# Performance work log

Measured on AMD Instinct MI355X. Metric: run time of the kernel, lower is better.

The kernel has to match this reference:

```python
import jax, jax.numpy as jnp
import numpy as np

N = 100000      # num nodes
E = 1600000     # num edges
D_IN = 128
D_OUT = 64
PRELU_INIT = 0.25


def setup_inputs() -> dict:
    key = jax.random.key(0)
    k1, k2, k3, k4, k5 = jax.random.split(key, 5)
    node_x = jax.random.normal(k1, (N, D_IN), dtype=jnp.float32)
    edge_rows = jax.random.randint(k2, (E,), 0, N, dtype=jnp.int32)
    edge_cols = jax.random.randint(k3, (E,), 0, N, dtype=jnp.int32)
    edge_vals = jax.random.uniform(k4, (E,), dtype=jnp.float32)
    # Xavier-uniform init for weights
    limit = float(np.sqrt(6.0 / (D_IN + D_OUT)))
    weights = jax.random.uniform(k5, (D_IN, D_OUT), dtype=jnp.float32,
                                 minval=-limit, maxval=limit)
    prelu_a = jnp.float32(PRELU_INIT)
    return {"node_x": node_x, "edge_rows": edge_rows, "edge_cols": edge_cols,
            "edge_vals": edge_vals, "weights": weights, "prelu_a": prelu_a}


def reference(node_x, edge_rows, edge_cols, edge_vals, weights, prelu_a):
    # Dense projection: [N, D_IN] @ [D_IN, D_OUT] -> [N, D_OUT]
    support = jnp.matmul(node_x, weights)
    # Sparse-dense matmul: output[r] = sum_{(r,c,v) in adj} v * support[c]
    messages = edge_vals[:, None] * support[edge_cols]  # [E, D_OUT]
    output = jax.ops.segment_sum(messages, edge_rows, num_segments=N)
    # PReLU with single learned scalar
    out = jnp.where(output > 0, output, prelu_a * output)
    return (out, support)
```

## Files before the change

kernel.cpp:

```cpp
#include <hip/hip_runtime.h>

#define N_NODES 100000
#define N_EDGES 1600000
#define D_IN    128
#define D_OUT   64

#define XT_STRIDE 260
#define NBUCKETS 1563
#define NBW 782
#define G 392
#define SLICE 4096
#define M_FLAT (NBUCKETS * G)
#define SCANA_BLOCKS 599
#define GEMM_BLOCKS 391
#define CAP 2048
typedef unsigned long long ull;
typedef unsigned int uint;

__global__ __launch_bounds__(256) void k_gemm_cnt(
    const float* __restrict__ x,
    const float* __restrict__ w,
    float* __restrict__ support,
    const int* __restrict__ rows,
    uint* __restrict__ S)
{
    __shared__ float wl[D_IN * D_OUT];
    __shared__ float xT[32 * XT_STRIDE];

    const int t = threadIdx.x;

    if (blockIdx.x >= GEMM_BLOCKS) {
        uint* hist = (uint*)wl;
        const int bid = blockIdx.x - GEMM_BLOCKS;
        const int b = (bid & 7) * 49 + (bid >> 3);
        for (int i = t; i < NBW; i += 256) hist[i] = 0u;
        __syncthreads();

        const int base = b * SLICE;
#pragma unroll
        for (int s2 = 0; s2 < 4; ++s2) {
            const int e = base + s2 * 1024 + t * 4;
            if (e < N_EDGES) {
                const int4 r4 = *(const int4*)&rows[e];
                atomicAdd(&hist[(uint)r4.x >> 7], 1u << ((((uint)r4.x >> 6) & 1) * 16));
                atomicAdd(&hist[(uint)r4.y >> 7], 1u << ((((uint)r4.y >> 6) & 1) * 16));
                atomicAdd(&hist[(uint)r4.z >> 7], 1u << ((((uint)r4.z >> 6) & 1) * 16));
                atomicAdd(&hist[(uint)r4.w >> 7], 1u << ((((uint)r4.w >> 6) & 1) * 16));
            }
        }
        __syncthreads();

        for (int i = t; i < NBUCKETS; i += 256)
            S[(size_t)i * G + b] = (hist[i >> 1] >> ((i & 1) * 16)) & 0xffffu;
        return;
    }

    const int tx = t & 7;
    const int ty = t >> 3;
    const long row0 = (long)blockIdx.x * 256;

    {
        const float4* wf  = (const float4*)w;
        float4*       wlf = (float4*)wl;
#pragma unroll
        for (int j = 0; j < 8; ++j)
            wlf[t + 256 * j] = wf[t + 256 * j];
    }

    float acc[8][8];
#pragma unroll
    for (int i = 0; i < 8; ++i)
#pragma unroll
        for (int j = 0; j < 8; ++j)
            acc[i][j] = 0.f;

    for (int kc = 0; kc < 4; ++kc) {
        const int k0 = kc * 32;
        __syncthreads();

        const int kk = tx * 4;
#pragma unroll
        for (int it = 0; it < 8; ++it) {
            const int  rg   = it * 32 + ty;
            const long grow = row0 + rg;
            float4 v = make_float4(0.f, 0.f, 0.f, 0.f);
            if (grow < N_NODES)
                v = *(const float4*)&x[grow * D_IN + k0 + kk];
            xT[(kk + 0) * XT_STRIDE + rg] = v.x;
            xT[(kk + 1) * XT_STRIDE + rg] = v.y;
            xT[(kk + 2) * XT_STRIDE + rg] = v.z;
            xT[(kk + 3) * XT_STRIDE + rg] = v.w;
        }
        __syncthreads();

#pragma unroll 8
        for (int k = 0; k < 32; ++k) {
            const float4 a0 = *(const float4*)&xT[k * XT_STRIDE + ty * 8];
            const float4 a1 = *(const float4*)&xT[k * XT_STRIDE + ty * 8 + 4];
            const float4 b0 = *(const float4*)&wl[(k0 + k) * D_OUT + tx * 8];
            const float4 b1 = *(const float4*)&wl[(k0 + k) * D_OUT + tx * 8 + 4];
            const float av[8] = {a0.x, a0.y, a0.z, a0.w, a1.x, a1.y, a1.z, a1.w};
            const float bv[8] = {b0.x, b0.y, b0.z, b0.w, b1.x, b1.y, b1.z, b1.w};
#pragma unroll
            for (int i = 0; i < 8; ++i)
#pragma unroll
                for (int j = 0; j < 8; ++j)
                    acc[i][j] = fmaf(av[i], bv[j], acc[i][j]);
        }
    }

#pragma unroll
    for (int i = 0; i < 8; ++i) {
        const long r = row0 + ty * 8 + i;
        if (r < N_NODES) {
            float4 o0 = make_float4(acc[i][0], acc[i][1], acc[i][2], acc[i][3]);
            float4 o1 = make_float4(acc[i][4], acc[i][5], acc[i][6], acc[i][7]);
            *(float4*)&support[r * D_OUT + tx * 8]     = o0;
            *(float4*)&support[r * D_OUT + tx * 8 + 4] = o1;
        }
    }
}

__global__ __launch_bounds__(256) void k_scanA(
    uint* __restrict__ S, uint* __restrict__ bsum)
{
    __shared__ uint s[256];
    const int t = threadIdx.x;
    const size_t base = (size_t)blockIdx.x * 1024 + (size_t)t * 4;
    uint4 v = make_uint4(0u, 0u, 0u, 0u);
    if (base < M_FLAT) v = *(const uint4*)&S[base];
    const uint tsum = v.x + v.y + v.z + v.w;
    s[t] = tsum;
    __syncthreads();
#pragma unroll
    for (int off = 1; off < 256; off <<= 1) {
        const uint add = (t >= off) ? s[t - off] : 0u;
        __syncthreads();
        s[t] += add;
        __syncthreads();
    }
    const uint eb = s[t] - tsum;
    if (t == 255) bsum[blockIdx.x] = s[255];
    if (base < M_FLAT) {
        uint4 o;
        o.x = eb; o.y = eb + v.x; o.z = o.y + v.y; o.w = o.z + v.z;
        *(uint4*)&S[base] = o;
    }
}

__global__ __launch_bounds__(256) void k_scatter(
    const int* __restrict__ rows, const int* __restrict__ cols,
    const float* __restrict__ vals, const uint* __restrict__ S,
    const uint* __restrict__ bsum, uint* __restrict__ bsum2,
    ull* __restrict__ pairs)
{
    __shared__ uint cur[NBUCKETS];
    __shared__ uint bs[SCANA_BLOCKS];
    __shared__ uint meta[256];
    const int t = threadIdx.x;
    const int bid = blockIdx.x;
    const int b = (bid & 7) * 49 + (bid >> 3);

    for (int i = t; i < SCANA_BLOCKS; i += 256) bs[i] = bsum[i];
    __syncthreads();

    uint carry = 0;
    for (int c0 = 0; c0 < SCANA_BLOCKS; c0 += 256) {
        const int i = c0 + t;
        const uint v = (i < SCANA_BLOCKS) ? bs[i] : 0u;
        meta[t] = v;
        __syncthreads();
#pragma unroll
        for (int off = 1; off < 256; off <<= 1) {
            const uint add = (t >= off) ? meta[t - off] : 0u;
            __syncthreads();
            meta[t] += add;
            __syncthreads();
        }
        if (i < SCANA_BLOCKS) bs[i] = carry + meta[t] - v;
        carry += meta[255];
        __syncthreads();
    }
    if (bid == 0)
        for (int i = t; i < SCANA_BLOCKS; i += 256) bsum2[i] = bs[i];

    for (int i = t; i < NBUCKETS; i += 256) {
        const size_t f = (size_t)i * G + b;
        cur[i] = S[f] + bs[f >> 10];
    }
    __syncthreads();

    const int base = b * SLICE;
#pragma unroll
    for (int s2 = 0; s2 < 4; ++s2) {
        const int e = base + s2 * 1024 + t * 4;
        if (e < N_EDGES) {
            const int4   r4 = *(const int4*)&rows[e];
            const int4   c4 = *(const int4*)&cols[e];
            const float4 v4 = *(const float4*)&vals[e];
            {
                const uint r = (uint)r4.x;
                const uint pos = atomicAdd(&cur[r >> 6], 1u);
                pairs[pos] = ((ull)__float_as_uint(v4.x) << 32)
                           | ((r & 63u) << 17) | (uint)c4.x;
            }
            {
                const uint r = (uint)r4.y;
                const uint pos = atomicAdd(&cur[r >> 6], 1u);
                pairs[pos] = ((ull)__float_as_uint(v4.y) << 32)
                           | ((r & 63u) << 17) | (uint)c4.y;
            }
            {
                const uint r = (uint)r4.z;
                const uint pos = atomicAdd(&cur[r >> 6], 1u);
                pairs[pos] = ((ull)__float_as_uint(v4.z) << 32)
                           | ((r & 63u) << 17) | (uint)c4.z;
            }
            {
                const uint r = (uint)r4.w;
                const uint pos = atomicAdd(&cur[r >> 6], 1u);
                pairs[pos] = ((ull)__float_as_uint(v4.w) << 32)
                           | ((r & 63u) << 17) | (uint)c4.w;
            }
        }
    }
}

__global__ __launch_bounds__(256) void k_bucket(
    const uint* __restrict__ S, const uint* __restrict__ bsum2,
    const ull* __restrict__ pairs, const float* __restrict__ support,
    const float* __restrict__ prelu_a, float* __restrict__ out)
{
    __shared__ ull srt[CAP];
    __shared__ uint h[64], ex[64], rowoff[64], cur[64];
    const int k = blockIdx.x;
    const int t = threadIdx.x, w = t >> 6, lane = t & 63;

    const size_t f0 = (size_t)k * G;
    const int beg = (int)(S[f0] + bsum2[f0 >> 10]);
    int end;
    if (k == NBUCKETS - 1) end = N_EDGES;
    else {
        const size_t f1 = f0 + G;
        end = (int)(S[f1] + bsum2[f1 >> 10]);
    }
    const int n = end - beg;
    const float a = prelu_a[0];

    if (t < 64) h[t] = 0u;
    __syncthreads();

    if (n <= CAP) {
        for (int i = t; i < n; i += 256)
            atomicAdd(&h[((uint)pairs[beg + i] >> 17) & 63u], 1u);
        __syncthreads();

        if (t < 64) ex[t] = h[t];
        __syncthreads();
#pragma unroll
        for (int off = 1; off < 64; off <<= 1) {
            const uint add = (t >= off && t < 64) ? ex[t - off] : 0u;
            __syncthreads();
            if (t < 64) ex[t] += add;
            __syncthreads();
        }
        if (t < 64) {
            rowoff[t] = ex[t] - h[t];
            cur[t]    = rowoff[t];
        }
        __syncthreads();

        for (int i = t; i < n; i += 256) {
            const ull p = pairs[beg + i];
            const uint pos = atomicAdd(&cur[((uint)p >> 17) & 63u], 1u);
            srt[pos] = p;
        }
        __syncthreads();

        for (int q = 0; q < 16; ++q) {
            const int rl  = w * 16 + q;
            const long row = (long)k * 64 + rl;
            if (row >= N_NODES) break;
            const int st  = (int)rowoff[rl];
            const int deg = (int)h[rl];

            float acc = 0.f;
            int j = 0;
            for (; j + 8 <= deg; j += 8) {
                ull p[8];
#pragma unroll
                for (int u = 0; u < 8; ++u) p[u] = srt[st + j + u];
                float sv[8];
#pragma unroll
                for (int u = 0; u < 8; ++u)
                    sv[u] = support[(size_t)((uint)p[u] & 0x1ffffu) * D_OUT + lane];
#pragma unroll
                for (int u = 0; u < 8; ++u)
                    acc = fmaf(__uint_as_float((uint)(p[u] >> 32)), sv[u], acc);
            }
            for (; j + 4 <= deg; j += 4) {
                ull p[4];
#pragma unroll
                for (int u = 0; u < 4; ++u) p[u] = srt[st + j + u];
                float sv[4];
#pragma unroll
                for (int u = 0; u < 4; ++u)
                    sv[u] = support[(size_t)((uint)p[u] & 0x1ffffu) * D_OUT + lane];
#pragma unroll
                for (int u = 0; u < 4; ++u)
                    acc = fmaf(__uint_as_float((uint)(p[u] >> 32)), sv[u], acc);
            }
            for (; j < deg; ++j) {
                const ull p = srt[st + j];
                acc = fmaf(__uint_as_float((uint)(p >> 32)),
                           support[(size_t)((uint)p & 0x1ffffu) * D_OUT + lane], acc);
            }
            out[row * D_OUT + lane] = acc > 0.f ? acc : a * acc;
        }
    } else {
        for (int q = 0; q < 16; ++q) {
            const int rl  = w * 16 + q;
            const long row = (long)k * 64 + rl;
            if (row >= N_NODES) break;
            float acc = 0.f;
            for (int i = 0; i < n; ++i) {
                const ull p = pairs[beg + i];
                if ((((uint)p >> 17) & 63u) == (uint)rl)
                    acc = fmaf(__uint_as_float((uint)(p >> 32)),
                               support[(size_t)((uint)p & 0x1ffffu) * D_OUT + lane],
                               acc);
            }
            out[row * D_OUT + lane] = acc > 0.f ? acc : a * acc;
        }
    }
}

extern "C" void kernel_launch(void* const* d_in, const int* in_sizes, int n_in,
                              void* d_out, int out_size, void* d_ws, size_t ws_size,
                              hipStream_t stream) {
    const float* x    = (const float*)d_in[0];
    const int*   rows = (const int*)d_in[1];
    const int*   cols = (const int*)d_in[2];
    const float* vals = (const float*)d_in[3];
    const float* w    = (const float*)d_in[4];
    const float* pa   = (const float*)d_in[5];

    float* out     = (float*)d_out;
    float* support = out + (size_t)N_NODES * D_OUT;

    uint* S     = (uint*)d_ws;
    uint* bsum  = S + (size_t)SCANA_BLOCKS * 1024;
    uint* bsum2 = bsum + 1024;
    ull*  pairs = (ull*)(bsum2 + 1024);

    k_gemm_cnt<<<GEMM_BLOCKS + G, 256, 0, stream>>>(x, w, support, rows, S);
    k_scanA   <<<SCANA_BLOCKS, 256, 0, stream>>>(S, bsum);
    k_scatter <<<G, 256, 0, stream>>>(rows, cols, vals, S, bsum, bsum2, pairs);
    k_bucket  <<<NBUCKETS, 256, 0, stream>>>(S, bsum2, pairs, support, pa, out);
}
```

Baseline: 229.2 us.

## Move GEMM from count kernel into scatter kernel to overlap with scatter

```diff
diff --git a/kernel.cpp b/kernel.cpp
--- a/kernel.cpp
+++ b/kernel.cpp
@@ -17,108 +17,31 @@
 typedef unsigned long long ull;
 typedef unsigned int uint;
 
-__global__ __launch_bounds__(256) void k_gemm_cnt(
-    const float* __restrict__ x,
-    const float* __restrict__ w,
-    float* __restrict__ support,
-    const int* __restrict__ rows,
-    uint* __restrict__ S)
+__global__ __launch_bounds__(256) void k_cnt(
+    const int* __restrict__ rows, uint* __restrict__ S)
 {
-    __shared__ float wl[D_IN * D_OUT];
-    __shared__ float xT[32 * XT_STRIDE];
-
+    __shared__ uint hist[NBW];
     const int t = threadIdx.x;
-
-    if (blockIdx.x >= GEMM_BLOCKS) {
-        uint* hist = (uint*)wl;
-        const int bid = blockIdx.x - GEMM_BLOCKS;
-        const int b = (bid & 7) * 49 + (bid >> 3);
-        for (int i = t; i < NBW; i += 256) hist[i] = 0u;
-        __syncthreads();
-
-        const int base = b * SLICE;
-#pragma unroll
-        for (int s2 = 0; s2 < 4; ++s2) {
-            const int e = base + s2 * 1024 + t * 4;
-            if (e < N_EDGES) {
-                const int4 r4 = *(const int4*)&rows[e];
-                atomicAdd(&hist[(uint)r4.x >> 7], 1u << ((((uint)r4.x >> 6) & 1) * 16));
-                atomicAdd(&hist[(uint)r4.y >> 7], 1u << ((((uint)r4.y >> 6) & 1) * 16));
-                atomicAdd(&hist[(uint)r4.z >> 7], 1u << ((((uint)r4.z >> 6) & 1) * 16));
-                atomicAdd(&hist[(uint)r4.w >> 7], 1u << ((((uint)r4.w >> 6) & 1) * 16));
-            }
-        }
-        __syncthreads();
-
-        for (int i = t; i < NBUCKETS; i += 256)
-            S[(size_t)i * G + b] = (hist[i >> 1] >> ((i & 1) * 16)) & 0xffffu;
-        return;
-    }
-
-    const int tx = t & 7;
-    const int ty = t >> 3;
-    const long row0 = (long)blockIdx.x * 256;
-
-    {
-        const float4* wf  = (const float4*)w;
-        float4*       wlf = (float4*)wl;
-#pragma unroll
-        for (int j = 0; j < 8; ++j)
-            wlf[t + 256 * j] = wf[t + 256 * j];
-    }
-
-    float acc[8][8];
-#pragma unroll
-    for (int i = 0; i < 8; ++i)
-#pragma unroll
-        for (int j = 0; j < 8; ++j)
-            acc[i][j] = 0.f;
-
-    for (int kc = 0; kc < 4; ++kc) {
-        const int k0 = kc * 32;
-        __syncthreads();
-
-        const int kk = tx * 4;
-#pragma unroll
-        for (int it = 0; it < 8; ++it) {
-            const int  rg   = it * 32 + ty;
-            const long grow = row0 + rg;
-            float4 v = make_float4(0.f, 0.f, 0.f, 0.f);
-            if (grow < N_NODES)
-                v = *(const float4*)&x[grow * D_IN + k0 + kk];
-            xT[(kk + 0) * XT_STRIDE + rg] = v.x;
-            xT[(kk + 1) * XT_STRIDE + rg] = v.y;
-            xT[(kk + 2) * XT_STRIDE + rg] = v.z;
-            xT[(kk + 3) * XT_STRIDE + rg] = v.w;
-        }
-        __syncthreads();
-
-#pragma unroll 8
-        for (int k = 0; k < 32; ++k) {
-            const float4 a0 = *(const float4*)&xT[k * XT_STRIDE + ty * 8];
-            const float4 a1 = *(const float4*)&xT[k * XT_STRIDE + ty * 8 + 4];
-            const float4 b0 = *(const float4*)&wl[(k0 + k) * D_OUT + tx * 8];
-            const float4 b1 = *(const float4*)&wl[(k0 + k) * D_OUT + tx * 8 + 4];
-            const float av[8] = {a0.x, a0.y, a0.z, a0.w, a1.x, a1.y, a1.z, a1.w};
-            const float bv[8] = {b0.x, b0.y, b0.z, b0.w, b1.x, b1.y, b1.z, b1.w};
-#pragma unroll
-            for (int i = 0; i < 8; ++i)
-#pragma unroll
-                for (int j = 0; j < 8; ++j)
-                    acc[i][j] = fmaf(av[i], bv[j], acc[i][j]);
-        }
-    }
-
-#pragma unroll
-    for (int i = 0; i < 8; ++i) {
-        const long r = row0 + ty * 8 + i;
-        if (r < N_NODES) {
-            float4 o0 = make_float4(acc[i][0], acc[i][1], acc[i][2], acc[i][3]);
-            float4 o1 = make_float4(acc[i][4], acc[i][5], acc[i][6], acc[i][7]);
-            *(float4*)&support[r * D_OUT + tx * 8]     = o0;
-            *(float4*)&support[r * D_OUT + tx * 8 + 4] = o1;
-        }
-    }
+    const int b = (blockIdx.x & 7) * 49 + (blockIdx.x >> 3);
+    for (int i = t; i < NBW; i += 256) hist[i] = 0u;
+    __syncthreads();
+
+    const int base = b * SLICE;
+#pragma unroll
+    for (int s2 = 0; s2 < 4; ++s2) {
+        const int e = base + s2 * 1024 + t * 4;
+        if (e < N_EDGES) {
+            const int4 r4 = *(const int4*)&rows[e];
+            atomicAdd(&hist[(uint)r4.x >> 7], 1u << ((((uint)r4.x >> 6) & 1) * 16));
+            atomicAdd(&hist[(uint)r4.y >> 7], 1u << ((((uint)r4.y >> 6) & 1) * 16));
+            atomicAdd(&hist[(uint)r4.z >> 7], 1u << ((((uint)r4.z >> 6) & 1) * 16));
+            atomicAdd(&hist[(uint)r4.w >> 7], 1u << ((((uint)r4.w >> 6) & 1) * 16));
+        }
+    }
+    __syncthreads();
+
+    for (int i = t; i < NBUCKETS; i += 256)
+        S[(size_t)i * G + b] = (hist[i >> 1] >> ((i & 1) * 16)) & 0xffffu;
 }
 
 __global__ __launch_bounds__(256) void k_scanA(
@@ -148,80 +71,157 @@
     }
 }
 
-__global__ __launch_bounds__(256) void k_scatter(
-    const int* __restrict__ rows, const int* __restrict__ cols,
-    const float* __restrict__ vals, const uint* __restrict__ S,
-    const uint* __restrict__ bsum, uint* __restrict__ bsum2,
-    ull* __restrict__ pairs)
+__global__ __launch_bounds__(256) void k_gemm_scatter(
+    const float* __restrict__ x, const float* __restrict__ w,
+    float* __restrict__ support, const int* __restrict__ rows,
+    const int* __restrict__ cols, const float* __restrict__ vals,
+    const uint* __restrict__ S, const uint* __restrict__ bsum,
+    uint* __restrict__ bsum2, ull* __restrict__ pairs)
 {
-    __shared__ uint cur[NBUCKETS];
-    __shared__ uint bs[SCANA_BLOCKS];
-    __shared__ uint meta[256];
+    __shared__ float wl[D_IN * D_OUT];
+    __shared__ float xT[32 * XT_STRIDE];
+
     const int t = threadIdx.x;
-    const int bid = blockIdx.x;
-    const int b = (bid & 7) * 49 + (bid >> 3);
-
-    for (int i = t; i < SCANA_BLOCKS; i += 256) bs[i] = bsum[i];
-    __syncthreads();
-
-    uint carry = 0;
-    for (int c0 = 0; c0 < SCANA_BLOCKS; c0 += 256) {
-        const int i = c0 + t;
-        const uint v = (i < SCANA_BLOCKS) ? bs[i] : 0u;
-        meta[t] = v;
-        __syncthreads();
-#pragma unroll
-        for (int off = 1; off < 256; off <<= 1) {
-            const uint add = (t >= off) ? meta[t - off] : 0u;
+    const int lane16 = blockIdx.x & 15;
+    const int grp    = blockIdx.x >> 4;
+
+    if (lane16 >= 8) {
+        const int sidx = grp * 8 + (lane16 - 8);
+        uint* cur  = (uint*)wl;
+        uint* bs   = (uint*)wl + 1600;
+        uint* meta = (uint*)wl + 2208;
+        const int b = (sidx & 7) * 49 + (sidx >> 3);
+
+        for (int i = t; i < SCANA_BLOCKS; i += 256) bs[i] = bsum[i];
+        __syncthreads();
+
+        uint carry = 0;
+        for (int c0 = 0; c0 < SCANA_BLOCKS; c0 += 256) {
+            const int i = c0 + t;
+            const uint v = (i < SCANA_BLOCKS) ? bs[i] : 0u;
+            meta[t] = v;
             __syncthreads();
-            meta[t] += add;
+#pragma unroll
+            for (int off = 1; off < 256; off <<= 1) {
+                const uint add = (t >= off) ? meta[t - off] : 0u;
+                __syncthreads();
+                meta[t] += add;
+                __syncthreads();
+            }
+            if (i < SCANA_BLOCKS) bs[i] = carry + meta[t] - v;
+            carry += meta[255];
             __syncthreads();
         }
-        if (i < SCANA_BLOCKS) bs[i] = carry + meta[t] - v;
-        carry += meta[255];
-        __syncthreads();
-    }
-    if (bid == 0)
-        for (int i = t; i < SCANA_BLOCKS; i += 256) bsum2[i] = bs[i];
-
-    for (int i = t; i < NBUCKETS; i += 256) {
-        const size_t f = (size_t)i * G + b;
-        cur[i] = S[f] + bs[f >> 10];
-    }
-    __syncthreads();
-
-    const int base = b * SLICE;
-#pragma unroll
-    for (int s2 = 0; s2 < 4; ++s2) {
-        const int e = base + s2 * 1024 + t * 4;
-        if (e < N_EDGES) {
-            const int4   r4 = *(const int4*)&rows[e];
-            const int4   c4 = *(const int4*)&cols[e];
-            const float4 v4 = *(const float4*)&vals[e];
-            {
-                const uint r = (uint)r4.x;
-                const uint pos = atomicAdd(&cur[r >> 6], 1u);
-                pairs[pos] = ((ull)__float_as_uint(v4.x) << 32)
-                           | ((r & 63u) << 17) | (uint)c4.x;
-            }
-            {
-                const uint r = (uint)r4.y;
-                const uint pos = atomicAdd(&cur[r >> 6], 1u);
-                pairs[pos] = ((ull)__float_as_uint(v4.y) << 32)
-                           | ((r & 63u) << 17) | (uint)c4.y;
-            }
-            {
-                const uint r = (uint)r4.z;
-                const uint pos = atomicAdd(&cur[r >> 6], 1u);
-                pairs[pos] = ((ull)__float_as_uint(v4.z) << 32)
-                           | ((r & 63u) << 17) | (uint)c4.z;
-            }
-            {
-                const uint r = (uint)r4.w;
-                const uint pos = atomicAdd(&cur[r >> 6], 1u);
-                pairs[pos] = ((ull)__float_as_uint(v4.w) << 32)
-                           | ((r & 63u) << 17) | (uint)c4.w;
-            }
+        if (sidx == 0)
+            for (int i = t; i < SCANA_BLOCKS; i += 256) bsum2[i] = bs[i];
+
+        for (int i = t; i < NBUCKETS; i += 256) {
+            const size_t f = (size_t)i * G + b;
+            cur[i] = S[f] + bs[f >> 10];
+        }
+        __syncthreads();
+
+        const int base = b * SLICE;
+#pragma unroll
+        for (int s2 = 0; s2 < 4; ++s2) {
+            const int e = base + s2 * 1024 + t * 4;
+            if (e < N_EDGES) {
+                const int4   r4 = *(const int4*)&rows[e];
+                const int4   c4 = *(const int4*)&cols[e];
+                const float4 v4 = *(const float4*)&vals[e];
+                {
+                    const uint r = (uint)r4.x;
+                    const uint pos = atomicAdd(&cur[r >> 6], 1u);
+                    pairs[pos] = ((ull)__float_as_uint(v4.x) << 32)
+                               | ((r & 63u) << 17) | (uint)c4.x;
+                }
+                {
+                    const uint r = (uint)r4.y;
+                    const uint pos = atomicAdd(&cur[r >> 6], 1u);
+                    pairs[pos] = ((ull)__float_as_uint(v4.y) << 32)
+                               | ((r & 63u) << 17) | (uint)c4.y;
+                }
+                {
+                    const uint r = (uint)r4.z;
+                    const uint pos = atomicAdd(&cur[r >> 6], 1u);
+                    pairs[pos] = ((ull)__float_as_uint(v4.z) << 32)
+                               | ((r & 63u) << 17) | (uint)c4.z;
+                }
+                {
+                    const uint r = (uint)r4.w;
+                    const uint pos = atomicAdd(&cur[r >> 6], 1u);
+                    pairs[pos] = ((ull)__float_as_uint(v4.w) << 32)
+                               | ((r & 63u) << 17) | (uint)c4.w;
+                }
+            }
+        }
+        return;
+    }
+
+    const int gid = grp * 8 + lane16;
+    if (gid >= GEMM_BLOCKS) return;
+    const int tx = t & 7;
+    const int ty = t >> 3;
+    const long row0 = (long)gid * 256;
+
+    {
+        const float4* wf  = (const float4*)w;
+        float4*       wlf = (float4*)wl;
+#pragma unroll
+        for (int j = 0; j < 8; ++j)
+            wlf[t + 256 * j] = wf[t + 256 * j];
+    }
+
+    float acc[8][8];
+#pragma unroll
+    for (int i = 0; i < 8; ++i)
+#pragma unroll
+        for (int j = 0; j < 8; ++j)
+            acc[i][j] = 0.f;
+
+    for (int kc = 0; kc < 4; ++kc) {
+        const int k0 = kc * 32;
+        __syncthreads();
+
+        const int kk = tx * 4;
+#pragma unroll
+        for (int it = 0; it < 8; ++it) {
+            const int  rg   = it * 32 + ty;
+            const long grow = row0 + rg;
+            float4 v = make_float4(0.f, 0.f, 0.f, 0.f);
+            if (grow < N_NODES)
+                v = *(const float4*)&x[grow * D_IN + k0 + kk];
+            xT[(kk + 0) * XT_STRIDE + rg] = v.x;
+            xT[(kk + 1) * XT_STRIDE + rg] = v.y;
+            xT[(kk + 2) * XT_STRIDE + rg] = v.z;
+            xT[(kk + 3) * XT_STRIDE + rg] = v.w;
+        }
+        __syncthreads();
+
+#pragma unroll 8
+        for (int k = 0; k < 32; ++k) {
+            const float4 a0 = *(const float4*)&xT[k * XT_STRIDE + ty * 8];
+            const float4 a1 = *(const float4*)&xT[k * XT_STRIDE + ty * 8 + 4];
+            const float4 b0 = *(const float4*)&wl[(k0 + k) * D_OUT + tx * 8];
+            const float4 b1 = *(const float4*)&wl[(k0 + k) * D_OUT + tx * 8 + 4];
+            const float av[8] = {a0.x, a0.y, a0.z, a0.w, a1.x, a1.y, a1.z, a1.w};
+            const float bv[8] = {b0.x, b0.y, b0.z, b0.w, b1.x, b1.y, b1.z, b1.w};
+#pragma unroll
+            for (int i = 0; i < 8; ++i)
+#pragma unroll
+                for (int j = 0; j < 8; ++j)
+                    acc[i][j] = fmaf(av[i], bv[j], acc[i][j]);
+        }
+    }
+
+#pragma unroll
+    for (int i = 0; i < 8; ++i) {
+        const long r = row0 + ty * 8 + i;
+        if (r < N_NODES) {
+            float4 o0 = make_float4(acc[i][0], acc[i][1], acc[i][2], acc[i][3]);
+            float4 o1 = make_float4(acc[i][4], acc[i][5], acc[i][6], acc[i][7]);
+            *(float4*)&support[r * D_OUT + tx * 8]     = o0;
+            *(float4*)&support[r * D_OUT + tx * 8 + 4] = o1;
         }
     }
 }
@@ -353,8 +353,9 @@
     uint* bsum2 = bsum + 1024;
     ull*  pairs = (ull*)(bsum2 + 1024);
 
-    k_gemm_cnt<<<GEMM_BLOCKS + G, 256, 0, stream>>>(x, w, support, rows, S);
-    k_scanA   <<<SCANA_BLOCKS, 256, 0, stream>>>(S, bsum);
-    k_scatter <<<G, 256, 0, stream>>>(rows, cols, vals, S, bsum, bsum2, pairs);
-    k_bucket  <<<NBUCKETS, 256, 0, stream>>>(S, bsum2, pairs, support, pa, out);
-}
+    k_cnt         <<<G, 256, 0, stream>>>(rows, S);
+    k_scanA       <<<SCANA_BLOCKS, 256, 0, stream>>>(S, bsum);
+    k_gemm_scatter<<<784, 256, 0, stream>>>(x, w, support, rows, cols, vals,
+                                            S, bsum, bsum2, pairs);
+    k_bucket      <<<NBUCKETS, 256, 0, stream>>>(S, bsum2, pairs, support, pa, out);
+}
```

Result: slower. 244.1 us (+6.5%).
